# Performance work log

Hardware: AMD Instinct MI355X
Metric: run time of the kernel (lower is better)

## Reference

```python
import jax, jax.numpy as jnp
import numpy as np

B, L, D_OUT, D_HIDDEN = 16, 4096, 1024, 512
MAX_PHASE = 6.28
R_MIN, R_MAX = 0.9, 0.999


def setup_inputs() -> dict:
    key = jax.random.key(0)
    ks = jax.random.split(key, 8)
    x = jax.random.normal(ks[0], (B, L, D_OUT), dtype=jnp.float32)
    # theta_init: log(max_phase * u)
    u_th = jax.random.uniform(ks[1], (D_HIDDEN,), dtype=jnp.float32)
    theta_log = jnp.log(MAX_PHASE * u_th)
    # nu_init: log(-0.5 * log(u * (r_max^2 - r_min^2) + r_min^2))
    u_nu = jax.random.uniform(ks[2], (D_HIDDEN,), dtype=jnp.float32)
    nu_log = jnp.log(-0.5 * jnp.log(u_nu * (R_MAX**2 - R_MIN**2) + R_MIN**2))
    # gamma_log_init from (nu_log, theta_log)
    diag_lambda = jnp.exp(-jnp.exp(nu_log) + 1j * jnp.exp(theta_log))
    gamma_log = jnp.log(jnp.sqrt(1.0 - jnp.abs(diag_lambda) ** 2))
    b_norm = jnp.sqrt(2.0 * D_OUT)
    c_norm = jnp.sqrt(float(D_HIDDEN))
    B_re = jax.random.normal(ks[3], (D_HIDDEN, D_OUT), dtype=jnp.float32) / b_norm
    B_im = jax.random.normal(ks[4], (D_HIDDEN, D_OUT), dtype=jnp.float32) / b_norm
    C_re = jax.random.normal(ks[5], (D_OUT, D_HIDDEN), dtype=jnp.float32) / c_norm
    C_im = jax.random.normal(ks[6], (D_OUT, D_HIDDEN), dtype=jnp.float32) / c_norm
    D = jax.random.normal(ks[7], (D_OUT,), dtype=jnp.float32)
    return {"x": x, "theta_log": theta_log, "nu_log": nu_log, "gamma_log": gamma_log,
            "B_re": B_re, "B_im": B_im, "C_re": C_re, "C_im": C_im, "D": D}


def _binop(q_i, q_j):
    # associative op for linear recurrence h_t = A_t * h_{t-1} + b_t (diagonal A)
    A_i, b_i = q_i
    A_j, b_j = q_j
    return (A_j * A_i, A_j * b_i + b_j)


def reference(x, theta_log, nu_log, gamma_log, B_re, B_im, C_re, C_im, D):
    diag_lambda = jnp.exp(-jnp.exp(nu_log) + 1j * jnp.exp(theta_log))  # (H,)
    B_norm = (B_re + 1j * B_im) * jnp.exp(gamma_log)[:, None]          # (H, D)
    C = C_re + 1j * C_im                                               # (D, H)
    # input projection: Bu_t = B_norm @ x_t -> (B, L, H) complex
    Bu = jnp.einsum('hd,bld->blh', B_norm, x.astype(B_norm.dtype))
    Lam = jnp.broadcast_to(diag_lambda, Bu.shape)
    # parallel scan over the sequence axis
    _, h = jax.lax.associative_scan(_binop, (Lam, Bu), axis=1)         # (B, L, H)
    # readout: y_t = Re[C h_t] + D * x_t
    y = jnp.einsum('oh,blh->blo', C, h).real + D * x
    return (y, h[:, -1])
```

## Files before the change

kernel.cpp:

```cpp
#include <hip/hip_runtime.h>

#define NB 16
#define NL 4096
#define NDO 1024
#define NH 512
#define NM (NB*NL)
#define NK 1024
#define NN 1024
#define CH 128
#define NCHUNK (NL/CH)
#define YCOUNT ((size_t)NM*NDO)
#define HCOUNT ((size_t)NB*NH)

typedef unsigned short u16;
typedef float f32x4 __attribute__((ext_vector_type(4)));
typedef unsigned int u32x4 __attribute__((ext_vector_type(4)));
typedef __bf16 bf16x8 __attribute__((ext_vector_type(8)));

__device__ __forceinline__ u16 f2bf(float f){
  unsigned u = __float_as_uint(f);
  unsigned r = u + 0x7fffu + ((u >> 16) & 1u);
  return (u16)(r >> 16);
}
__device__ __forceinline__ float bf2f(u16 v){ return __uint_as_float(((unsigned)v) << 16); }
__device__ __forceinline__ unsigned pack2(float a, float b){
  return (unsigned)f2bf(a) | ((unsigned)f2bf(b) << 16);
}

__device__ __forceinline__ void gld_lds16(const u16* g, u16* l){
  __builtin_amdgcn_global_load_lds(
      (const __attribute__((address_space(1))) unsigned int*)g,
      (__attribute__((address_space(3))) unsigned int*)l,
      16, 0, 0);
}


__global__ void prep_w1(const float* __restrict__ Bre, const float* __restrict__ Bim,
                        const float* __restrict__ gl, u16* __restrict__ W1){
  int i = blockIdx.x * blockDim.x + threadIdx.x;
  if (i >= NH * NDO) return;
  int h = i / NDO, d = i % NDO;
  float g = expf(gl[h]);
  W1[(size_t)h * NK + d]        = f2bf(Bre[i] * g);
  W1[(size_t)(NH + h) * NK + d] = f2bf(Bim[i] * g);
}

__global__ void prep_w2(const float* __restrict__ Cre, const float* __restrict__ Cim,
                        u16* __restrict__ W2){
  int i = blockIdx.x * blockDim.x + threadIdx.x;
  if (i >= NDO * NH) return;
  int o = i / NH, k = i % NH;
  W2[(size_t)o * NK + k]      = f2bf(Cre[i]);
  W2[(size_t)o * NK + NH + k] = f2bf(-Cim[i]);
}

__global__ void prep_lam(const float* __restrict__ theta_log, const float* __restrict__ nu_log,
                         float* __restrict__ lam){
  int h = threadIdx.x;
  if (h >= NH) return;
  float nu = expf(nu_log[h]);
  float th = expf(theta_log[h]);
  float mag = expf(-nu);
  float lre = mag * cosf(th), lim = mag * sinf(th);
  double pre = (double)lre, pim = (double)lim;
  #pragma unroll
  for (int s = 0; s < 7; s++){
    double nr = pre*pre - pim*pim;
    double ni = 2.0*pre*pim;
    pre = nr; pim = ni;
  }
  lam[h]        = lre;
  lam[NH + h]   = lim;
  lam[2*NH + h] = (float)pre;
  lam[3*NH + h] = (float)pim;
}

__global__ __launch_bounds__(256) void convert_x(const float* __restrict__ X, u16* __restrict__ Xb){
  size_t i = ((size_t)blockIdx.x * 256 + threadIdx.x) * 8;
  f32x4 a = *(const f32x4*)(X + i);
  f32x4 b = *(const f32x4*)(X + i + 4);
  u32x4 p;
  p[0] = pack2(a[0], a[1]); p[1] = pack2(a[2], a[3]);
  p[2] = pack2(b[0], b[1]); p[3] = pack2(b[2], b[3]);
  *(u32x4*)(Xb + i) = p;
}

template<int MODE>
__global__ __launch_bounds__(256) void gemm_m97(const u16* __restrict__ A,
                                                const u16* __restrict__ W,
                                                const float* __restrict__ X,
                                                const float* __restrict__ Dv,
                                                u16* __restrict__ outB,
                                                float* __restrict__ outF){
  __shared__ __align__(16) u16 Alds[128][32];
  __shared__ __align__(16) u16 Blds[128][32];
  const int tid = threadIdx.x;
  const int bid = blockIdx.x;
  const int lid = (bid & 7) * 512 + (bid >> 3);
  const int m0 = (lid >> 3) << 7;
  const int n0 = (lid & 7) << 7;
  const int w = tid >> 6, lane = tid & 63;
  const int wm = w >> 1, wn = w & 1;

  const int sr = lane >> 2;
  const int sc = (lane & 3) << 3;
  const u16* ag = A + (size_t)(m0 + w*32 + sr) * NK + sc;
  const u16* bg = W + (size_t)(n0 + w*32 + sr) * NK + sc;
  u16* al0 = &Alds[w*32][0];
  u16* al1 = &Alds[w*32 + 16][0];
  u16* bl0 = &Blds[w*32][0];
  u16* bl1 = &Blds[w*32 + 16][0];

  f32x4 acc[4][4];
#pragma unroll
  for (int i = 0; i < 4; i++)
#pragma unroll
    for (int j = 0; j < 4; j++) acc[i][j] = (f32x4){0.f,0.f,0.f,0.f};

  const int klane = (lane >> 4) << 3;
  const int rowa = wm*64 + (lane & 15);
  const int rowb = wn*64 + (lane & 15);

  for (int k0 = 0; k0 < NK; k0 += 32) {
    gld_lds16(ag + k0,           al0);
    gld_lds16(ag + k0 + 16*NK,   al1);
    gld_lds16(bg + k0,           bl0);
    gld_lds16(bg + k0 + 16*NK,   bl1);
    __syncthreads();
    bf16x8 af[4], bv[4];
#pragma unroll
    for (int i = 0; i < 4; i++){
      af[i] = *(const bf16x8*)&Alds[rowa + i*16][klane];
      bv[i] = *(const bf16x8*)&Blds[rowb + i*16][klane];
    }
#pragma unroll
    for (int i = 0; i < 4; i++)
#pragma unroll
      for (int j = 0; j < 4; j++)
        acc[i][j] = __builtin_amdgcn_mfma_f32_16x16x32_bf16(af[i], bv[j], acc[i][j], 0, 0, 0);
    __syncthreads();
  }

  const int r0 = (lane >> 4) << 2;
  const int col = lane & 15;
#pragma unroll
  for (int i = 0; i < 4; i++){
    int gm = m0 + wm*64 + i*16 + r0;
#pragma unroll
    for (int j = 0; j < 4; j++){
      int gn = n0 + wn*64 + j*16 + col;
      if constexpr (MODE == 0) {
#pragma unroll
        for (int r = 0; r < 4; r++)
          outB[(size_t)(gm + r) * NN + gn] = f2bf(acc[i][j][r]);
      } else {
        float dv = Dv[gn];
#pragma unroll
        for (int r = 0; r < 4; r++){
          size_t oidx = (size_t)(gm + r) * NDO + gn;
          outF[oidx] = acc[i][j][r] + dv * X[oidx];
        }
      }
    }
  }
}


__global__ __launch_bounds__(256) void gemm1_legacy(const float* __restrict__ X,
                                                    const u16* __restrict__ W1,
                                                    u16* __restrict__ Bu){
  __shared__ __align__(16) u16 Alds[128][32];
  __shared__ __align__(16) u16 Blds[128][32];
  const int tid = threadIdx.x;
  const int bid = blockIdx.x;
  const int lid = (bid & 7) * 512 + (bid >> 3);
  const int m0 = (lid >> 3) << 7;
  const int n0 = (lid & 7) << 7;
  const int w = tid >> 6, lane = tid & 63;
  const int wm = w >> 1, wn = w & 1;
  f32x4 acc[4][4];
#pragma unroll
  for (int i = 0; i < 4; i++)
#pragma unroll
    for (int j = 0; j < 4; j++) acc[i][j] = (f32x4){0.f,0.f,0.f,0.f};

  const int srow = tid >> 1;
  const int skseg = (tid & 1) << 4;
  const float* xp = X + (size_t)(m0 + srow) * NK + skseg;
  const u16*  wp  = W1 + (size_t)(n0 + srow) * NK + skseg;

  const int klane = (lane >> 4) << 3;
  const int rowa = wm*64 + (lane & 15);
  const int rowb = wn*64 + (lane & 15);

  for (int k0 = 0; k0 < NK; k0 += 32) {
    __syncthreads();
    f32x4 v0 = *(const f32x4*)(xp + k0 + 0);
    f32x4 v1 = *(const f32x4*)(xp + k0 + 4);
    f32x4 v2 = *(const f32x4*)(xp + k0 + 8);
    f32x4 v3 = *(const f32x4*)(xp + k0 + 12);
    u32x4 q0 = *(const u32x4*)(wp + k0);
    u32x4 q1 = *(const u32x4*)(wp + k0 + 8);
    u32x4 p0, p1;
    p0[0] = pack2(v0[0], v0[1]); p0[1] = pack2(v0[2], v0[3]);
    p0[2] = pack2(v1[0], v1[1]); p0[3] = pack2(v1[2], v1[3]);
    p1[0] = pack2(v2[0], v2[1]); p1[1] = pack2(v2[2], v2[3]);
    p1[2] = pack2(v3[0], v3[1]); p1[3] = pack2(v3[2], v3[3]);
    *(u32x4*)&Alds[srow][skseg]     = p0;
    *(u32x4*)&Alds[srow][skseg + 8] = p1;
    *(u32x4*)&Blds[srow][skseg]     = q0;
    *(u32x4*)&Blds[srow][skseg + 8] = q1;
    __syncthreads();
    bf16x8 af[4], bv[4];
#pragma unroll
    for (int i = 0; i < 4; i++){
      af[i] = *(const bf16x8*)&Alds[rowa + i*16][klane];
      bv[i] = *(const bf16x8*)&Blds[rowb + i*16][klane];
    }
#pragma unroll
    for (int i = 0; i < 4; i++)
#pragma unroll
      for (int j = 0; j < 4; j++)
        acc[i][j] = __builtin_amdgcn_mfma_f32_16x16x32_bf16(af[i], bv[j], acc[i][j], 0, 0, 0);
  }

  const int r0 = (lane >> 4) << 2;
  const int col = lane & 15;
#pragma unroll
  for (int i = 0; i < 4; i++){
    int gm = m0 + wm*64 + i*16 + r0;
#pragma unroll
    for (int j = 0; j < 4; j++){
      int gn = n0 + wn*64 + j*16 + col;
#pragma unroll
      for (int r = 0; r < 4; r++)
        Bu[(size_t)(gm + r) * NN + gn] = f2bf(acc[i][j][r]);
    }
  }
}


__global__ __launch_bounds__(512) void scan_carry(const u16* __restrict__ Bu,
                                                  const float* __restrict__ lam,
                                                  float* __restrict__ carry){
  const int h = threadIdx.x;
  const int bc = blockIdx.x;
  const int b = bc / NCHUNK, c = bc % NCHUNK;
  const float lre = lam[h], lim = lam[NH + h];
  float hre = 0.f, him = 0.f;
  size_t base = (size_t)(b * NL + c * CH) * NN;
  for (int j = 0; j < CH; j++){
    float bre = bf2f(Bu[base + (size_t)j*NN + h]);
    float bim = bf2f(Bu[base + (size_t)j*NN + NH + h]);
    float nre = lre*hre - lim*him + bre;
    float nim = lre*him + lim*hre + bim;
    hre = nre; him = nim;
  }
  size_t ci = ((size_t)bc * NH + h) * 2;
  carry[ci] = hre; carry[ci + 1] = him;
}

__global__ __launch_bounds__(512) void scan_combine(const float* __restrict__ carry,
                                                    const float* __restrict__ lam,
                                                    float* __restrict__ hstart){
  const int h = threadIdx.x;
  const int b = blockIdx.x;
  const float Pre = lam[2*NH + h], Pim = lam[3*NH + h];
  float are = 0.f, aim = 0.f;
  for (int c = 0; c < NCHUNK; c++){
    size_t idx = ((size_t)(b * NCHUNK + c) * NH + h) * 2;
    hstart[idx] = are; hstart[idx + 1] = aim;
    float cre = carry[idx], cim = carry[idx + 1];
    float nre = Pre*are - Pim*aim + cre;
    float nim = Pre*aim + Pim*are + cim;
    are = nre; aim = nim;
  }
}

__global__ __launch_bounds__(512) void scan_fixup(u16* __restrict__ Bu,
                                                  const float* __restrict__ lam,
                                                  const float* __restrict__ hstart,
                                                  float* __restrict__ out, int out_size){
  const int h = threadIdx.x;
  const int bc = blockIdx.x;
  const int b = bc / NCHUNK, c = bc % NCHUNK;
  const float lre = lam[h], lim = lam[NH + h];
  size_t si = ((size_t)bc * NH + h) * 2;
  const float sre = hstart[si], sim = hstart[si + 1];
  float hre = 0.f, him = 0.f;
  float pre = lre, pim = lim;
  size_t base = (size_t)(b * NL + c * CH) * NN;
  for (int j = 0; j < CH; j++){
    float bre = bf2f(Bu[base + (size_t)j*NN + h]);
    float bim = bf2f(Bu[base + (size_t)j*NN + NH + h]);
    float nre = lre*hre - lim*him + bre;
    float nim = lre*him + lim*hre + bim;
    hre = nre; him = nim;
    float vre = hre + pre*sre - pim*sim;
    float vim = him + pre*sim + pim*sre;
    Bu[base + (size_t)j*NN + h]      = f2bf(vre);
    Bu[base + (size_t)j*NN + NH + h] = f2bf(vim);
    if (c == NCHUNK - 1 && j == CH - 1){
      size_t ore_i = YCOUNT + (size_t)b * NH + h;
      size_t oim_i = YCOUNT + HCOUNT + (size_t)b * NH + h;
      if (ore_i < (size_t)out_size) out[ore_i] = vre;
      if (oim_i < (size_t)out_size) out[oim_i] = vim;
    }
    float qre = pre*lre - pim*lim;
    float qim = pre*lim + pim*lre;
    pre = qre; pim = qim;
  }
}


extern "C" void kernel_launch(void* const* d_in, const int* in_sizes, int n_in,
                              void* d_out, int out_size, void* d_ws, size_t ws_size,
                              hipStream_t stream) {
  const float* x         = (const float*)d_in[0];
  const float* theta_log = (const float*)d_in[1];
  const float* nu_log    = (const float*)d_in[2];
  const float* gamma_log = (const float*)d_in[3];
  const float* Bre       = (const float*)d_in[4];
  const float* Bim       = (const float*)d_in[5];
  const float* Cre       = (const float*)d_in[6];
  const float* Cim       = (const float*)d_in[7];
  const float* Dv        = (const float*)d_in[8];
  float* out = (float*)d_out;
  char* ws = (char*)d_ws;

  u16*   W1     = (u16*)(ws);
  u16*   W2     = (u16*)(ws + (2u << 20));
  float* lam    = (float*)(ws + (4u << 20));
  float* carry  = (float*)(ws + (5u << 20));
  float* hstart = (float*)(ws + (7u << 20));
  u16*   Bu     = (u16*)(ws + (16u << 20));
  u16*   Xb     = (u16*)(ws + (144u << 20));
  size_t need_base = (16u << 20) + (size_t)NM * NN * 2;
  size_t need_fast = need_base + (size_t)NM * NK * 2;
  if (ws_size < need_base) return;
  const bool fast = (ws_size >= need_fast);

  prep_w1<<<(NH * NDO + 255) / 256, 256, 0, stream>>>(Bre, Bim, gamma_log, W1);
  prep_w2<<<(NDO * NH + 255) / 256, 256, 0, stream>>>(Cre, Cim, W2);
  prep_lam<<<1, 512, 0, stream>>>(theta_log, nu_log, lam);

  if (fast) {
    convert_x<<<(int)(YCOUNT / (256*8)), 256, 0, stream>>>(x, Xb);
    gemm_m97<0><<<4096, 256, 0, stream>>>(Xb, W1, nullptr, nullptr, Bu, nullptr);
  } else {
    gemm1_legacy<<<4096, 256, 0, stream>>>(x, W1, Bu);
  }

  scan_carry<<<NB * NCHUNK, 512, 0, stream>>>(Bu, lam, carry);
  scan_combine<<<NB, 512, 0, stream>>>(carry, lam, hstart);
  scan_fixup<<<NB * NCHUNK, 512, 0, stream>>>(Bu, lam, hstart, out, out_size);

  gemm_m97<1><<<4096, 256, 0, stream>>>(Bu, W2, x, Dv, nullptr, out);
}
```

Before: 606.1 us.

## Double-buffer LDS tiles in bf16 GEMMs to overlap loads with MFMA

Both GEMM kernels now use two LDS buffers for the A and B tiles. The next K-slice is loaded directly into the alternate buffer while MFMAs run on the current one, and the loop needs only one wait plus barrier per iteration instead of two syncthreads. The goal is to hide global-to-LDS load latency behind matrix compute. In exchange, LDS use per block doubles, which may reduce occupancy. The single barrier per step is only safe if every wave has finished reading a buffer before it is overwritten two iterations later.

```diff
diff --git a/kernel.cpp b/kernel.cpp
--- a/kernel.cpp
+++ b/kernel.cpp
@@ -86,14 +86,14 @@
 }
 
 template<int MODE>
-__global__ __launch_bounds__(256) void gemm_m97(const u16* __restrict__ A,
+__global__ __launch_bounds__(256) void gemm_2ph(const u16* __restrict__ A,
                                                 const u16* __restrict__ W,
                                                 const float* __restrict__ X,
                                                 const float* __restrict__ Dv,
                                                 u16* __restrict__ outB,
                                                 float* __restrict__ outF){
-  __shared__ __align__(16) u16 Alds[128][32];
-  __shared__ __align__(16) u16 Blds[128][32];
+  __shared__ __align__(16) u16 Alds[2][128][32];
+  __shared__ __align__(16) u16 Blds[2][128][32];
   const int tid = threadIdx.x;
   const int bid = blockIdx.x;
   const int lid = (bid & 7) * 512 + (bid >> 3);
@@ -106,10 +106,6 @@
   const int sc = (lane & 3) << 3;
   const u16* ag = A + (size_t)(m0 + w*32 + sr) * NK + sc;
   const u16* bg = W + (size_t)(n0 + w*32 + sr) * NK + sc;
-  u16* al0 = &Alds[w*32][0];
-  u16* al1 = &Alds[w*32 + 16][0];
-  u16* bl0 = &Blds[w*32][0];
-  u16* bl1 = &Blds[w*32 + 16][0];
 
   f32x4 acc[4][4];
 #pragma unroll
@@ -121,25 +117,42 @@
   const int rowa = wm*64 + (lane & 15);
   const int rowb = wn*64 + (lane & 15);
 
-  for (int k0 = 0; k0 < NK; k0 += 32) {
-    gld_lds16(ag + k0,           al0);
-    gld_lds16(ag + k0 + 16*NK,   al1);
-    gld_lds16(bg + k0,           bl0);
-    gld_lds16(bg + k0 + 16*NK,   bl1);
-    __syncthreads();
-    bf16x8 af[4], bv[4];
-#pragma unroll
-    for (int i = 0; i < 4; i++){
-      af[i] = *(const bf16x8*)&Alds[rowa + i*16][klane];
-      bv[i] = *(const bf16x8*)&Blds[rowb + i*16][klane];
-    }
-#pragma unroll
-    for (int i = 0; i < 4; i++)
-#pragma unroll
-      for (int j = 0; j < 4; j++)
-        acc[i][j] = __builtin_amdgcn_mfma_f32_16x16x32_bf16(af[i], bv[j], acc[i][j], 0, 0, 0);
-    __syncthreads();
-  }
+#define STAGE(buf, k0) do {                                   \
+    gld_lds16(ag + (k0),           &Alds[buf][w*32][0]);      \
+    gld_lds16(ag + (k0) + 16*NK,   &Alds[buf][w*32+16][0]);   \
+    gld_lds16(bg + (k0),           &Blds[buf][w*32][0]);      \
+    gld_lds16(bg + (k0) + 16*NK,   &Blds[buf][w*32+16][0]);   \
+  } while(0)
+
+#define COMPUTE(buf) do {                                           \
+    bf16x8 af[4], bv[4];                                            \
+    _Pragma("unroll")                                               \
+    for (int i = 0; i < 4; i++){                                    \
+      af[i] = *(const bf16x8*)&Alds[buf][rowa + i*16][klane];       \
+      bv[i] = *(const bf16x8*)&Blds[buf][rowb + i*16][klane];       \
+    }                                                               \
+    _Pragma("unroll")                                               \
+    for (int i = 0; i < 4; i++)                                     \
+      _Pragma("unroll")                                             \
+      for (int j = 0; j < 4; j++)                                   \
+        acc[i][j] = __builtin_amdgcn_mfma_f32_16x16x32_bf16(af[i], bv[j], acc[i][j], 0, 0, 0); \
+  } while(0)
+
+  STAGE(0, 0);
+  asm volatile("s_waitcnt vmcnt(0)" ::: "memory");
+  __builtin_amdgcn_s_barrier();
+
+  for (int t = 0; t < (NK/32) - 1; ++t) {
+    const int cur = t & 1;
+    STAGE(cur ^ 1, (t + 1) * 32);
+    COMPUTE(cur);
+    asm volatile("s_waitcnt vmcnt(0)" ::: "memory");
+    __builtin_amdgcn_s_barrier();
+  }
+  COMPUTE((NK/32 - 1) & 1);
+
+#undef STAGE
+#undef COMPUTE
 
   const int r0 = (lane >> 4) << 2;
   const int col = lane & 15;
@@ -346,7 +359,7 @@
 
   if (fast) {
     convert_x<<<(int)(YCOUNT / (256*8)), 256, 0, stream>>>(x, Xb);
-    gemm_m97<0><<<4096, 256, 0, stream>>>(Xb, W1, nullptr, nullptr, Bu, nullptr);
+    gemm_2ph<0><<<4096, 256, 0, stream>>>(Xb, W1, nullptr, nullptr, Bu, nullptr);
   } else {
     gemm1_legacy<<<4096, 256, 0, stream>>>(x, W1, Bu);
   }
@@ -355,5 +368,5 @@
   scan_combine<<<NB, 512, 0, stream>>>(carry, lam, hstart);
   scan_fixup<<<NB * NCHUNK, 512, 0, stream>>>(Bu, lam, hstart, out, out_size);
 
-  gemm_m97<1><<<4096, 256, 0, stream>>>(Bu, W2, x, Dv, nullptr, out);
-}
+  gemm_2ph<1><<<4096, 256, 0, stream>>>(Bu, W2, x, Dv, nullptr, out);
+}
```

After: 732.5 us. +20.9%, slower.

## Use 256x256 double-buffered swizzled-LDS GEMM tiles and bf16 x in readout epilogue

Applied to the files above, without the earlier changes.

Replaces the 128x128, K=32 single-buffered GEMM with a 512-thread kernel that computes 256x256 output tiles over K=64 stages. LDS tiles are double-buffered and XOR-swizzled, so global-to-LDS loads for the next stage overlap MFMA work on the current one. The larger tile raises data reuse per byte loaded. In the fast path, the readout epilogue now reads the already-converted bf16 copy of x for the D*x skip term instead of fp32 x, which halves that traffic but lowers the precision of the residual. The new kernel uses much more LDS and registers per block, so occupancy drops.

```diff
diff --git a/kernel.cpp b/kernel.cpp
--- a/kernel.cpp
+++ b/kernel.cpp
@@ -85,80 +85,140 @@
   *(u32x4*)(Xb + i) = p;
 }
 
+
+__device__ __forceinline__ void stage_tile(const u16* Ag, const u16* Bg, int kt,
+                                           u16 (&AB)[256][64], u16 (&BB)[256][64], int w){
+  const u16* a = Ag + (size_t)kt * 64;
+  const u16* b = Bg + (size_t)kt * 64;
+  #pragma unroll
+  for (int s = 0; s < 4; s++){
+    gld_lds16(a + (size_t)s * 8 * NK, &AB[w*32 + s*8][0]);
+    gld_lds16(b + (size_t)s * 8 * NK, &BB[w*32 + s*8][0]);
+  }
+}
+
+__device__ __forceinline__ void compute_tile(const u16 (&AB)[256][64], const u16 (&BB)[256][64],
+                                             f32x4 (&acc)[8][4], int wr, int wc,
+                                             int c15, int sw0, int sw1){
+  #pragma unroll
+  for (int mh = 0; mh < 2; mh++){
+    bf16x8 af[4][2];
+    #pragma unroll
+    for (int i = 0; i < 4; i++){
+      const u16* p = &AB[wr*128 + mh*64 + i*16 + c15][0];
+      af[i][0] = *(const bf16x8*)(p + sw0);
+      af[i][1] = *(const bf16x8*)(p + sw1);
+    }
+    #pragma unroll
+    for (int nh = 0; nh < 2; nh++){
+      bf16x8 bv[2][2];
+      #pragma unroll
+      for (int j = 0; j < 2; j++){
+        const u16* p = &BB[wc*64 + nh*32 + j*16 + c15][0];
+        bv[j][0] = *(const bf16x8*)(p + sw0);
+        bv[j][1] = *(const bf16x8*)(p + sw1);
+      }
+      #pragma unroll
+      for (int i = 0; i < 4; i++)
+        #pragma unroll
+        for (int j = 0; j < 2; j++){
+          acc[mh*4+i][nh*2+j] = __builtin_amdgcn_mfma_f32_16x16x32_bf16(af[i][0], bv[j][0], acc[mh*4+i][nh*2+j], 0, 0, 0);
+          acc[mh*4+i][nh*2+j] = __builtin_amdgcn_mfma_f32_16x16x32_bf16(af[i][1], bv[j][1], acc[mh*4+i][nh*2+j], 0, 0, 0);
+        }
+    }
+  }
+}
+
 template<int MODE>
-__global__ __launch_bounds__(256) void gemm_m97(const u16* __restrict__ A,
+__global__ __launch_bounds__(512) void gemm_256(const u16* __restrict__ A,
                                                 const u16* __restrict__ W,
-                                                const float* __restrict__ X,
+                                                const float* __restrict__ Xf,
+                                                const u16* __restrict__ Xh,
                                                 const float* __restrict__ Dv,
                                                 u16* __restrict__ outB,
                                                 float* __restrict__ outF){
-  __shared__ __align__(16) u16 Alds[128][32];
-  __shared__ __align__(16) u16 Blds[128][32];
+  __shared__ __align__(16) u16 A0[256][64];
+  __shared__ __align__(16) u16 B0[256][64];
+  __shared__ __align__(16) u16 A1[256][64];
+  __shared__ __align__(16) u16 B1[256][64];
   const int tid = threadIdx.x;
   const int bid = blockIdx.x;
-  const int lid = (bid & 7) * 512 + (bid >> 3);
-  const int m0 = (lid >> 3) << 7;
-  const int n0 = (lid & 7) << 7;
+  const int lid = (bid & 7) * 128 + (bid >> 3);
+  const int m0 = (lid >> 2) << 8;
+  const int n0 = (lid & 3) << 8;
   const int w = tid >> 6, lane = tid & 63;
-  const int wm = w >> 1, wn = w & 1;
-
-  const int sr = lane >> 2;
-  const int sc = (lane & 3) << 3;
-  const u16* ag = A + (size_t)(m0 + w*32 + sr) * NK + sc;
-  const u16* bg = W + (size_t)(n0 + w*32 + sr) * NK + sc;
-  u16* al0 = &Alds[w*32][0];
-  u16* al1 = &Alds[w*32 + 16][0];
-  u16* bl0 = &Blds[w*32][0];
-  u16* bl1 = &Blds[w*32 + 16][0];
-
-  f32x4 acc[4][4];
-#pragma unroll
-  for (int i = 0; i < 4; i++)
-#pragma unroll
-    for (int j = 0; j < 4; j++) acc[i][j] = (f32x4){0.f,0.f,0.f,0.f};
-
-  const int klane = (lane >> 4) << 3;
-  const int rowa = wm*64 + (lane & 15);
-  const int rowb = wn*64 + (lane & 15);
-
-  for (int k0 = 0; k0 < NK; k0 += 32) {
-    gld_lds16(ag + k0,           al0);
-    gld_lds16(ag + k0 + 16*NK,   al1);
-    gld_lds16(bg + k0,           bl0);
-    gld_lds16(bg + k0 + 16*NK,   bl1);
-    __syncthreads();
-    bf16x8 af[4], bv[4];
-#pragma unroll
-    for (int i = 0; i < 4; i++){
-      af[i] = *(const bf16x8*)&Alds[rowa + i*16][klane];
-      bv[i] = *(const bf16x8*)&Blds[rowb + i*16][klane];
-    }
-#pragma unroll
-    for (int i = 0; i < 4; i++)
-#pragma unroll
-      for (int j = 0; j < 4; j++)
-        acc[i][j] = __builtin_amdgcn_mfma_f32_16x16x32_bf16(af[i], bv[j], acc[i][j], 0, 0, 0);
-    __syncthreads();
-  }
-
-  const int r0 = (lane >> 4) << 2;
-  const int col = lane & 15;
-#pragma unroll
-  for (int i = 0; i < 4; i++){
-    int gm = m0 + wm*64 + i*16 + r0;
-#pragma unroll
-    for (int j = 0; j < 4; j++){
-      int gn = n0 + wn*64 + j*16 + col;
+  const int wr = w >> 2, wc = w & 3;
+
+  const int grow = lane >> 3;
+  const int gcol = ((lane & 7) ^ grow) << 3;
+  const u16* Ag = A + (size_t)(m0 + w*32 + grow) * NK + gcol;
+  const u16* Bg = W + (size_t)(n0 + w*32 + grow) * NK + gcol;
+
+  const int c15 = lane & 15;
+  const int qb  = lane >> 4;
+  const int sw0 = ((qb    ) ^ (lane & 7)) << 3;
+  const int sw1 = ((qb | 4) ^ (lane & 7)) << 3;
+
+  f32x4 acc[8][4];
+  #pragma unroll
+  for (int m = 0; m < 8; m++)
+    #pragma unroll
+    for (int n = 0; n < 4; n++) acc[m][n] = (f32x4){0.f,0.f,0.f,0.f};
+
+#define LGKM0() asm volatile("s_waitcnt lgkmcnt(0)" ::: "memory")
+#define VM0()   asm volatile("s_waitcnt vmcnt(0)" ::: "memory")
+#define BAR()   __builtin_amdgcn_s_barrier()
+
+  stage_tile(Ag, Bg, 0, A0, B0, w);
+  VM0();
+  BAR();
+
+  #pragma unroll 1
+  for (int kt = 0; kt < NK/64; kt += 2){
+    stage_tile(Ag, Bg, kt + 1, A1, B1, w);
+    compute_tile(A0, B0, acc, wr, wc, c15, sw0, sw1);
+    LGKM0();
+    BAR();
+    VM0();
+    BAR();
+    if (kt + 2 < NK/64){
+      stage_tile(Ag, Bg, kt + 2, A0, B0, w);
+      compute_tile(A1, B1, acc, wr, wc, c15, sw0, sw1);
+      LGKM0(); BAR();
+      VM0();  BAR();
+    } else {
+      compute_tile(A1, B1, acc, wr, wc, c15, sw0, sw1);
+    }
+  }
+
+#undef LGKM0
+#undef VM0
+#undef BAR
+
+  const int r4 = (lane >> 4) << 2;
+  #pragma unroll
+  for (int m = 0; m < 8; m++){
+    int gm = m0 + wr*128 + m*16 + r4;
+    #pragma unroll
+    for (int n = 0; n < 4; n++){
+      int gn = n0 + wc*64 + n*16 + c15;
       if constexpr (MODE == 0) {
-#pragma unroll
+        #pragma unroll
         for (int r = 0; r < 4; r++)
-          outB[(size_t)(gm + r) * NN + gn] = f2bf(acc[i][j][r]);
+          outB[(size_t)(gm + r) * NN + gn] = f2bf(acc[m][n][r]);
+      } else if constexpr (MODE == 1) {
+        float dv = Dv[gn];
+        #pragma unroll
+        for (int r = 0; r < 4; r++){
+          size_t oidx = (size_t)(gm + r) * NDO + gn;
+          outF[oidx] = acc[m][n][r] + dv * Xf[oidx];
+        }
       } else {
         float dv = Dv[gn];
-#pragma unroll
+        #pragma unroll
         for (int r = 0; r < 4; r++){
           size_t oidx = (size_t)(gm + r) * NDO + gn;
-          outF[oidx] = acc[i][j][r] + dv * X[oidx];
+          outF[oidx] = acc[m][n][r] + dv * bf2f(Xh[oidx]);
         }
       }
     }
@@ -344,9 +404,11 @@
   prep_w2<<<(NDO * NH + 255) / 256, 256, 0, stream>>>(Cre, Cim, W2);
   prep_lam<<<1, 512, 0, stream>>>(theta_log, nu_log, lam);
 
+  const int g256 = (NM / 256) * (NN / 256);
+
   if (fast) {
     convert_x<<<(int)(YCOUNT / (256*8)), 256, 0, stream>>>(x, Xb);
-    gemm_m97<0><<<4096, 256, 0, stream>>>(Xb, W1, nullptr, nullptr, Bu, nullptr);
+    gemm_256<0><<<g256, 512, 0, stream>>>(Xb, W1, nullptr, nullptr, nullptr, Bu, nullptr);
   } else {
     gemm1_legacy<<<4096, 256, 0, stream>>>(x, W1, Bu);
   }
@@ -355,5 +417,9 @@
   scan_combine<<<NB, 512, 0, stream>>>(carry, lam, hstart);
   scan_fixup<<<NB * NCHUNK, 512, 0, stream>>>(Bu, lam, hstart, out, out_size);
 
-  gemm_m97<1><<<4096, 256, 0, stream>>>(Bu, W2, x, Dv, nullptr, out);
-}
+  if (fast) {
+    gemm_256<2><<<g256, 512, 0, stream>>>(Bu, W2, nullptr, Xb, Dv, nullptr, out);
+  } else {
+    gemm_256<1><<<g256, 512, 0, stream>>>(Bu, W2, x, nullptr, Dv, nullptr, out);
+  }
+}
```

Result: slower. 1.262 ms (+108.2%).
